# Optimization experiments

Measured on AMD Instinct MI355X. Metric: run time of the kernel, lower is better.

The kernel has to match this reference:

```python
import jax, jax.numpy as jnp
import numpy as np


def gcn_conv(x, edge_index, W, b):
    """GCNConv with add_self_loops + symmetric deg^-1/2 normalization, aggr='add'."""
    n = x.shape[0]
    self_loops = jnp.arange(n, dtype=edge_index.dtype)
    row = jnp.concatenate([edge_index[0], self_loops])  # source (j)
    col = jnp.concatenate([edge_index[1], self_loops])  # target (i)
    h = x @ W + b  # [N, out]
    deg = jax.ops.segment_sum(jnp.ones(row.shape, dtype=h.dtype), row, num_segments=n)
    dinv = jnp.where(deg > 0, deg ** -0.5, 0.0)
    norm = dinv[row] * dinv[col]  # [E+N]
    # out[i] = sum_{e: col_e = i} norm_e * h[row_e]
    return jax.ops.segment_sum(norm[:, None] * h[row], col, num_segments=n)


def setup_inputs() -> dict:
    key = jax.random.key(0)
    ks = jax.random.split(key, 5)
    N, E, D, K, C = 50000, 800000, 64, 500, 64
    x = jax.random.normal(ks[0], (N, D), dtype=jnp.float32)
    edge_index = jax.random.randint(ks[1], (2, E), 0, N, dtype=jnp.int32)
    W_embed = jax.random.normal(ks[2], (D, C), dtype=jnp.float32) * 0.1
    b_embed = jnp.zeros((C,), dtype=jnp.float32)
    W_assign = jax.random.normal(ks[3], (D, K), dtype=jnp.float32) * 0.1
    b_assign = jnp.zeros((K,), dtype=jnp.float32)
    return {"x": x, "edge_index": edge_index, "W_embed": W_embed, "b_embed": b_embed,
            "W_assign": W_assign, "b_assign": b_assign}


def reference(x, edge_index, W_embed, b_embed, W_assign, b_assign):
    n = x.shape[0]
    Z = gcn_conv(x, edge_index, W_embed, b_embed)                      # [N, C]
    S = jax.nn.softmax(gcn_conv(x, edge_index, W_assign, b_assign), -1)  # [N, K]
    next_X = S.T @ Z                                                    # [K, C]
    # next_A = S^T A S with A the (multi-)adjacency of the ORIGINAL edge_index
    # (to_dense_adj adds 1 at A[row_e, col_e]); computed sparsely:
    row, col = edge_index[0], edge_index[1]
    AS = jax.ops.segment_sum(S[col], row, num_segments=n)               # [N, K] = A @ S
    next_A = S.T @ AS                                                   # [K, K]
    return next_X, next_A
```

## Files before the change

### kernel.cpp

```cpp
#include <hip/hip_runtime.h>
#include <hip/hip_bf16.h>
#include <math.h>

#define DD 64
#define KK 500
#define KPAD 512
#define NPAD 50048
#define NS 50176
#define SLOTS 128
#define NBUCK 196
#define BCAP 6144

typedef __attribute__((ext_vector_type(8))) short bf16x8;
typedef __attribute__((ext_vector_type(4))) float f32x4;

#if defined(__has_builtin)
#if __has_builtin(__builtin_amdgcn_cvt_pk_f32_fp8) && __has_builtin(__builtin_amdgcn_cvt_pk_fp8_f32)
#define HAS_FP8_CVT 1
#endif
#endif

#ifdef HAS_FP8_CVT
#define F8_INV (1.0f / 256.f)
#else
#define F8_INV 0x1p112f
#endif

__device__ inline unsigned short f2bf(float f) {
    unsigned u = __float_as_uint(f);
    u += 0x7fffu + ((u >> 16) & 1u);
    return (unsigned short)(u >> 16);
}
__device__ inline unsigned packbf(float lo, float hi) {
    return ((unsigned)f2bf(hi) << 16) | (unsigned)f2bf(lo);
}
__device__ inline float bf2f(unsigned short h) {
    return __uint_as_float((unsigned)h << 16);
}

__device__ inline void gload_lds16(const void* g, void* l) {
    __builtin_amdgcn_global_load_lds(
        (const __attribute__((address_space(1))) unsigned int*)g,
        (__attribute__((address_space(3))) unsigned int*)l, 16, 0, 0);
}

#ifndef HAS_FP8_CVT
__device__ inline float f8bits(unsigned b) {
    return __uint_as_float(((b & 0x80u) << 24) | ((b & 0x7fu) << 20));
}
__device__ inline unsigned f32_to_fp8_slow(float f) {
    unsigned sgn = (__float_as_uint(f) >> 24) & 0x80u;
    float af = fabsf(f);
    if (!(af > 0.f)) return sgn;
    if (af >= 448.f) return sgn | 0x7E;
    int e; frexpf(af, &e);
    int E = e - 1 + 7;
    if (E < 1) { unsigned q = (unsigned)rintf(ldexpf(af, 9)); return sgn | q; }
    unsigned q = (unsigned)rintf(ldexpf(af, 10 - E));
    if (q >= 16) { q = 8; E++; }
    if (E > 15 || (E == 15 && q - 8 >= 7)) return sgn | 0x7E;
    return sgn | ((unsigned)E << 3) | (q - 8);
}
#endif

__device__ inline void accf8v4(float* a, uint4 v) {
#ifdef HAS_FP8_CVT
    auto f0 = __builtin_amdgcn_cvt_pk_f32_fp8(v.x, false);
    a[0] += f0[0]; a[1] += f0[1];
    auto f1 = __builtin_amdgcn_cvt_pk_f32_fp8(v.x, true);
    a[2] += f1[0]; a[3] += f1[1];
    auto f2 = __builtin_amdgcn_cvt_pk_f32_fp8(v.y, false);
    a[4] += f2[0]; a[5] += f2[1];
    auto f3 = __builtin_amdgcn_cvt_pk_f32_fp8(v.y, true);
    a[6] += f3[0]; a[7] += f3[1];
    auto f4 = __builtin_amdgcn_cvt_pk_f32_fp8(v.z, false);
    a[8] += f4[0]; a[9] += f4[1];
    auto f5 = __builtin_amdgcn_cvt_pk_f32_fp8(v.z, true);
    a[10] += f5[0]; a[11] += f5[1];
    auto f6 = __builtin_amdgcn_cvt_pk_f32_fp8(v.w, false);
    a[12] += f6[0]; a[13] += f6[1];
    auto f7 = __builtin_amdgcn_cvt_pk_f32_fp8(v.w, true);
    a[14] += f7[0]; a[15] += f7[1];
#else
    a[0]  += f8bits(v.x & 0xff);         a[1]  += f8bits((v.x >> 8) & 0xff);
    a[2]  += f8bits((v.x >> 16) & 0xff); a[3]  += f8bits((v.x >> 24) & 0xff);
    a[4]  += f8bits(v.y & 0xff);         a[5]  += f8bits((v.y >> 8) & 0xff);
    a[6]  += f8bits((v.y >> 16) & 0xff); a[7]  += f8bits((v.y >> 24) & 0xff);
    a[8]  += f8bits(v.z & 0xff);         a[9]  += f8bits((v.z >> 8) & 0xff);
    a[10] += f8bits((v.z >> 16) & 0xff); a[11] += f8bits((v.z >> 24) & 0xff);
    a[12] += f8bits(v.w & 0xff);         a[13] += f8bits((v.w >> 8) & 0xff);
    a[14] += f8bits((v.w >> 16) & 0xff); a[15] += f8bits((v.w >> 24) & 0xff);
#endif
}

__device__ inline void accbf4(float* a, uint2 v) {
    a[0] += __uint_as_float(v.x << 16);
    a[1] += __uint_as_float(v.x & 0xffff0000u);
    a[2] += __uint_as_float(v.y << 16);
    a[3] += __uint_as_float(v.y & 0xffff0000u);
}

__global__ void __launch_bounds__(256) binA_kernel(
        const int* __restrict__ rowv, const int* __restrict__ colv,
        int* __restrict__ bcurC, int* __restrict__ bcurR,
        int* __restrict__ bstoreC, unsigned char* __restrict__ bstoreR, int E) {
    __shared__ int hc[NBUCK], hr[NBUCK], baseC[NBUCK], baseR[NBUCK];
    int t = threadIdx.x;
    if (t < NBUCK) { hc[t] = 0; hr[t] = 0; }
    __syncthreads();
    int e0 = blockIdx.x * 1024 + t * 4;
    int r[4], c[4];
#pragma unroll
    for (int i = 0; i < 4; ++i) {
        int e = e0 + i;
        if (e < E) {
            r[i] = rowv[e];
            c[i] = colv[e];
            atomicAdd(&hc[c[i] >> 8], 1);
            atomicAdd(&hr[r[i] >> 8], 1);
        } else {
            r[i] = -1; c[i] = -1;
        }
    }
    __syncthreads();
    if (t < NBUCK) {
        baseC[t] = atomicAdd(&bcurC[t], hc[t]);
        baseR[t] = atomicAdd(&bcurR[t], hr[t]);
        hc[t] = 0; hr[t] = 0;
    }
    __syncthreads();
#pragma unroll
    for (int i = 0; i < 4; ++i) {
        if (r[i] >= 0) {
            int bc = c[i] >> 8;
            int oc = baseC[bc] + atomicAdd(&hc[bc], 1);
            if (oc < BCAP) bstoreC[bc * BCAP + oc] = (r[i] << 8) | (c[i] & 255);
            int br = r[i] >> 8;
            int orr = baseR[br] + atomicAdd(&hr[br], 1);
            if (orr < BCAP) bstoreR[br * BCAP + orr] = (unsigned char)(r[i] & 255);
        }
    }
}

__global__ void __launch_bounds__(256) buildcsr_kernel(
        const int* __restrict__ bcurC, const int* __restrict__ bstoreC,
        int* __restrict__ esrc, int* __restrict__ degc, int n) {
    __shared__ int cur[256];
    int b = blockIdx.x, t = threadIdx.x;
    cur[t] = 0;
    __syncthreads();
    int cnt = min(bcurC[b], BCAP);
    const int* src = bstoreC + b * BCAP;
    for (int i = t; i < cnt; i += 256) {
        int packed = src[i];
        int cl = packed & 255, rr = packed >> 8;
        int p = atomicAdd(&cur[cl], 1);
        if (p < SLOTS) esrc[((size_t)(b * 256 + cl) << 7) + p] = rr;
    }
    __syncthreads();
    int node = b * 256 + t;
    if (node < n) degc[node] = min(cur[t], SLOTS);
}

__global__ void __launch_bounds__(256) rowdeg_kernel(
        const int* __restrict__ bcurR, const unsigned char* __restrict__ bstoreR,
        float* __restrict__ dinv, int n) {
    __shared__ int cnt[256];
    int b = blockIdx.x, t = threadIdx.x;
    cnt[t] = 0;
    __syncthreads();
    int c = min(bcurR[b], BCAP);
    const unsigned char* src = bstoreR + b * BCAP;
    for (int i = t; i < c; i += 256) {
        atomicAdd(&cnt[src[i]], 1);
    }
    __syncthreads();
    int node = b * 256 + t;
    if (node < n) dinv[node] = 1.0f / sqrtf((float)(cnt[t] + 1));
}

__global__ void prep_kernel(const float* __restrict__ x, const float* __restrict__ dinv,
                            unsigned short* __restrict__ xb,
                            const float* __restrict__ Wa, const float* __restrict__ We,
                            unsigned short* __restrict__ WaT, unsigned short* __restrict__ WeT,
                            int n16) {
    int idx = blockIdx.x * blockDim.x + threadIdx.x;
    if (idx < n16) {
        int i = idx >> 4;
        float di = dinv[i];
        float4 v = ((const float4*)x)[idx];
        uint2 o;
        o.x = packbf(di * v.x, di * v.y);
        o.y = packbf(di * v.z, di * v.w);
        ((uint2*)xb)[idx] = o;
        return;
    }
    int j = idx - n16;
    if (j < KPAD * 64) {
        int c = j >> 6, d = j & 63;
        float v = (c < KK) ? Wa[(size_t)d * KK + c] : 0.f;
        WaT[j] = f2bf(v);
    } else if (j < (KPAD + DD) * 64) {
        int k = j - KPAD * 64;
        int c = k >> 6, d = k & 63;
        WeT[k] = f2bf(We[(size_t)d * 64 + c]);
    }
}

__global__ void agg_kernel(const unsigned short* __restrict__ xb, const float* __restrict__ dinv,
                           const int* __restrict__ degc, const int* __restrict__ esrc,
                           float* __restrict__ t, unsigned short* __restrict__ ub, int n) {
    int wv = (blockIdx.x * blockDim.x + threadIdx.x) >> 6;
    int ln = threadIdx.x & 63;
    int g = ln >> 4, q = ln & 15;
    if (wv >= NPAD) return;
    if (wv >= n) {
        if (g == 0) ((uint2*)ub)[(size_t)wv * 16 + q] = make_uint2(0u, 0u);
        return;
    }
    const uint2* X2 = (const uint2*)xb;
    float ac[4] = {0.f, 0.f, 0.f, 0.f};
    float ts = 0.f;
    if (g == 0) {
        uint2 v = X2[(size_t)wv * 16 + q];
        accbf4(ac, v);
    }
    int p = wv << 7;
    int pend = p + degc[wv];
    for (; p + 7 < pend; p += 8) {
        int s0 = esrc[p + g];
        int s1 = esrc[p + 4 + g];
        uint2 v0 = X2[(size_t)s0 * 16 + q];
        uint2 v1 = X2[(size_t)s1 * 16 + q];
        float w0 = dinv[s0], w1 = dinv[s1];
        accbf4(ac, v0); accbf4(ac, v1);
        ts += w0 + w1;
    }
    for (; p + 3 < pend; p += 4) {
        int s = esrc[p + g];
        uint2 v = X2[(size_t)s * 16 + q];
        ts += dinv[s];
        accbf4(ac, v);
    }
    if (g < pend - p) {
        int s = esrc[p + g];
        uint2 v = X2[(size_t)s * 16 + q];
        ts += dinv[s];
        accbf4(ac, v);
    }
#pragma unroll
    for (int j = 0; j < 4; ++j) {
        ac[j] += __shfl_xor(ac[j], 16, 64);
        ac[j] += __shfl_xor(ac[j], 32, 64);
    }
    ts += __shfl_xor(ts, 16, 64);
    ts += __shfl_xor(ts, 32, 64);
    if (g == 0) {
        uint2 o;
        o.x = packbf(ac[0], ac[1]);
        o.y = packbf(ac[2], ac[3]);
        ((uint2*)ub)[(size_t)wv * 16 + q] = o;
        if (q == 0) t[wv] = dinv[wv] + ts;
    }
}

#define F8ROW 520
__global__ void __launch_bounds__(256) fused_s3_kernel(
        const unsigned short* __restrict__ ub, const unsigned short* __restrict__ WaT,
        const unsigned short* __restrict__ WeT,
        const float* __restrict__ ba, const float* __restrict__ be,
        const float* __restrict__ dinv, const float* __restrict__ tsum,
        unsigned short* __restrict__ S_T, unsigned char* __restrict__ Sf8,
        unsigned short* __restrict__ Z_T, int n) {
    __shared__ float bs[512];
    __shared__ float bes[64];
    __shared__ float wmax[4][16];
    __shared__ float wsum[4][16];
    __shared__ unsigned char f8[16 * F8ROW];
    int t = threadIdx.x;
    int n0 = blockIdx.x * 16;
    {
        float b0 = (t * 2     < KK) ? ba[t * 2]     : 0.f;
        float b1 = (t * 2 + 1 < KK) ? ba[t * 2 + 1] : 0.f;
        bs[t * 2] = b0; bs[t * 2 + 1] = b1;
        if (t < 64) bes[t] = be[t];
    }
    __syncthreads();
    int wv = t >> 6, ln = t & 63;
    int nl = ln & 15;
    int g  = ln >> 4;
    int node = n0 + nl;
    int kb = wv * 128;
    float sd = (node < n) ? dinv[node] : 0.f;
    float st = (node < n) ? tsum[node] : 0.f;
    const unsigned short* brow = ub + (size_t)node * 64;
    bf16x8 bf0 = *(const bf16x8*)&brow[g * 8];
    bf16x8 bf1 = *(const bf16x8*)&brow[32 + g * 8];
    f32x4 acc[8];
#pragma unroll
    for (int mt = 0; mt < 8; ++mt) {
        const unsigned short* arow = WaT + (size_t)(kb + mt * 16 + nl) * 64;
        bf16x8 af0 = *(const bf16x8*)&arow[g * 8];
        bf16x8 af1 = *(const bf16x8*)&arow[32 + g * 8];
        f32x4 a = __builtin_amdgcn_mfma_f32_16x16x32_bf16(af0, bf0, (f32x4){0.f,0.f,0.f,0.f}, 0, 0, 0);
        acc[mt] = __builtin_amdgcn_mfma_f32_16x16x32_bf16(af1, bf1, a, 0, 0, 0);
    }
    float m = -1e30f;
#pragma unroll
    for (int mt = 0; mt < 8; ++mt) {
#pragma unroll
        for (int r = 0; r < 4; ++r) {
            int cl = kb + mt * 16 + g * 4 + r;
            float L = sd * (acc[mt][r] + st * bs[cl]);
            if (cl >= KK) L = -1e30f;
            acc[mt][r] = L;
            m = fmaxf(m, L);
        }
    }
    m = fmaxf(m, __shfl_xor(m, 16, 64));
    m = fmaxf(m, __shfl_xor(m, 32, 64));
    if (g == 0) wmax[wv][nl] = m;
    __syncthreads();
    m = fmaxf(fmaxf(wmax[0][nl], wmax[1][nl]), fmaxf(wmax[2][nl], wmax[3][nl]));
    float ssum = 0.f;
#pragma unroll
    for (int mt = 0; mt < 8; ++mt) {
#pragma unroll
        for (int r = 0; r < 4; ++r) {
            float e = expf(acc[mt][r] - m);
            acc[mt][r] = e;
            ssum += e;
        }
    }
    ssum += __shfl_xor(ssum, 16, 64);
    ssum += __shfl_xor(ssum, 32, 64);
    if (g == 0) wsum[wv][nl] = ssum;
    __syncthreads();
    float tot = (wsum[0][nl] + wsum[1][nl]) + (wsum[2][nl] + wsum[3][nl]);
    float rs = (node < n) ? (1.0f / tot) : 0.f;
    float sc = 256.f * rs;
    unsigned char* frow = &f8[nl * F8ROW];
#pragma unroll
    for (int mt = 0; mt < 8; ++mt) {
#pragma unroll
        for (int r = 0; r < 4; ++r) {
            int cl = kb + mt * 16 + g * 4 + r;
            S_T[(size_t)cl * NPAD + node] = f2bf(acc[mt][r] * rs);
        }
#ifdef HAS_FP8_CVT
        int pk = __builtin_amdgcn_cvt_pk_fp8_f32(acc[mt][0] * sc, acc[mt][1] * sc, 0, false);
        pk     = __builtin_amdgcn_cvt_pk_fp8_f32(acc[mt][2] * sc, acc[mt][3] * sc, pk, true);
#else
        int pk = (int)(f32_to_fp8_slow(acc[mt][0]*sc) | (f32_to_fp8_slow(acc[mt][1]*sc) << 8) |
                       (f32_to_fp8_slow(acc[mt][2]*sc) << 16) | (f32_to_fp8_slow(acc[mt][3]*sc) << 24));
#endif
        *(unsigned*)&frow[kb + mt * 16 + g * 4] = (unsigned)pk;
    }
    {
        const unsigned short* arow = WeT + (size_t)(wv * 16 + nl) * 64;
        bf16x8 af0 = *(const bf16x8*)&arow[g * 8];
        bf16x8 af1 = *(const bf16x8*)&arow[32 + g * 8];
        f32x4 a = __builtin_amdgcn_mfma_f32_16x16x32_bf16(af0, bf0, (f32x4){0.f,0.f,0.f,0.f}, 0, 0, 0);
        a = __builtin_amdgcn_mfma_f32_16x16x32_bf16(af1, bf1, a, 0, 0, 0);
#pragma unroll
        for (int r = 0; r < 4; ++r) {
            int ch = wv * 16 + g * 4 + r;
            float z = sd * (a[r] + st * bes[ch]);
            Z_T[(size_t)ch * NPAD + node] = f2bf(z);
        }
    }
    __syncthreads();
#pragma unroll
    for (int h = 0; h < 2; ++h) {
        int idx = t + h * 256;
        int row = idx >> 5;
        int off = (idx & 31) * 16;
        uint4 vv = *(const uint4*)&f8[row * F8ROW + off];
        int grow = n0 + row;
        if (grow < n) *(uint4*)&Sf8[(size_t)grow * KPAD + off] = vv;
    }
}

#define GT_ROWS 32
__global__ void __launch_bounds__(512) g_agg_t_kernel(
        const unsigned char* __restrict__ Sf8, const int* __restrict__ degc,
        const int* __restrict__ esrc, unsigned short* __restrict__ G_T, int n) {
    __shared__ unsigned short tl[GT_ROWS * 520];
    __shared__ int nextrow;
    int base = blockIdx.x * GT_ROWS;
    int ln = threadIdx.x & 63;
    int half = ln >> 5, lc = ln & 31;
    if (threadIdx.x == 0) nextrow = 0;
    __syncthreads();
    const uint4* S4 = (const uint4*)Sf8;
    const float inv = F8_INV;
    while (true) {
        int r = 0;
        if (ln == 0) r = atomicAdd(&nextrow, 1);
        r = __shfl(r, 0, 64);
        if (r >= GT_ROWS) break;
        int node = base + r;
        float a[16];
#pragma unroll
        for (int j = 0; j < 16; ++j) a[j] = 0.f;
        if (node < n) {
            int p = node << 7;
            int pend = p + degc[node];
            for (; p + 7 < pend; p += 8) {
                int s0 = esrc[p + half];
                int s1 = esrc[p + 2 + half];
                int s2 = esrc[p + 4 + half];
                int s3 = esrc[p + 6 + half];
                uint4 v0 = S4[(size_t)s0 * 32 + lc];
                uint4 v1 = S4[(size_t)s1 * 32 + lc];
                uint4 v2 = S4[(size_t)s2 * 32 + lc];
                uint4 v3 = S4[(size_t)s3 * 32 + lc];
                accf8v4(a, v0); accf8v4(a, v1); accf8v4(a, v2); accf8v4(a, v3);
            }
            for (; p + 1 < pend; p += 2) {
                int s = esrc[p + half];
                uint4 v = S4[(size_t)s * 32 + lc];
                accf8v4(a, v);
            }
            if (p < pend && half == 0) {
                int s = esrc[p];
                uint4 v = S4[(size_t)s * 32 + lc];
                accf8v4(a, v);
            }
        }
#pragma unroll
        for (int j = 0; j < 16; ++j) a[j] += __shfl_xor(a[j], 32, 64);
        uint4 o;
        if (half == 0) {
            o.x = packbf(a[0] * inv, a[1] * inv);
            o.y = packbf(a[2] * inv, a[3] * inv);
            o.z = packbf(a[4] * inv, a[5] * inv);
            o.w = packbf(a[6] * inv, a[7] * inv);
        } else {
            o.x = packbf(a[8]  * inv, a[9]  * inv);
            o.y = packbf(a[10] * inv, a[11] * inv);
            o.z = packbf(a[12] * inv, a[13] * inv);
            o.w = packbf(a[14] * inv, a[15] * inv);
        }
        *(uint4*)&tl[r * 520 + lc * 16 + half * 8] = o;
    }
    __syncthreads();
    {
        int k = threadIdx.x;
        unsigned wb[8];
#pragma unroll
        for (int j = 0; j < 8; ++j) {
            unsigned short lo = tl[(2 * j)     * 520 + k];
            unsigned short hi = tl[(2 * j + 1) * 520 + k];
            wb[j] = ((unsigned)hi << 16) | (unsigned)lo;
        }
        unsigned wc[8];
#pragma unroll
        for (int j = 0; j < 8; ++j) {
            unsigned short lo = tl[(16 + 2 * j) * 520 + k];
            unsigned short hi = tl[(17 + 2 * j) * 520 + k];
            wc[j] = ((unsigned)hi << 16) | (unsigned)lo;
        }
        size_t ob = (size_t)k * NPAD + base;
        *(uint4*)&G_T[ob]      = make_uint4(wb[0], wb[1], wb[2], wb[3]);
        *(uint4*)&G_T[ob + 8]  = make_uint4(wb[4], wb[5], wb[6], wb[7]);
        *(uint4*)&G_T[ob + 16] = make_uint4(wc[0], wc[1], wc[2], wc[3]);
        *(uint4*)&G_T[ob + 24] = make_uint4(wc[4], wc[5], wc[6], wc[7]);
    }
}

#define CPITCH 128
__global__ void __launch_bounds__(256) mfma_comb_kernel(
        const unsigned short* __restrict__ S_T, const unsigned short* __restrict__ G_T,
        const unsigned short* __restrict__ Z_T,
        float* __restrict__ partialA, float* __restrict__ partialX, int nPer) {
    __shared__ unsigned short Al[128 * 64];
    __shared__ unsigned short Bl[128 * 64];
    const int bid = blockIdx.x;
    const int kws = (bid & 7) * 115 + (bid >> 3);
    const int tile = kws % 20;
    const int zz   = kws / 20;
    const int t = threadIdx.x;
    const int ln = t & 63, wv = t >> 6;
    const int wa = (wv & 1) * 64, wb = (wv >> 1) * 64;
    const int lm = ln & 15, lk = (ln >> 4) * 8;
    const int nbeg = zz * nPer;
    const int nend = min(nbeg + nPer, NPAD);
    const bool isA = (tile < 16);
    const unsigned short* Ap = isA ? G_T : S_T;
    const unsigned short* Bp = isA ? S_T : Z_T;
    const int a0 = isA ? (tile >> 2) * 128 : (tile - 16) * 128;
    const int b0 = isA ? (tile & 3) * 128 : 0;
    float* op = isA ? (partialA + (size_t)zz * 512 * 512)
                    : (partialX + (size_t)zz * 512 * 128);
    const int ostride = isA ? 512 : 128;
    const int srow = ln >> 3;
    const int schunk = ((ln & 7) * 16) ^ (srow << 4);
    f32x4 acc[4][4];
#pragma unroll
    for (int i = 0; i < 4; ++i)
#pragma unroll
        for (int j = 0; j < 4; ++j) acc[i][j] = (f32x4){0.f, 0.f, 0.f, 0.f};
    for (int nb = nbeg; nb < nend; nb += 64) {
        __syncthreads();
#pragma unroll
        for (int j = 0; j < 4; ++j) {
            int rbase = (j * 4 + wv) * 8;
            int row = rbase + srow;
            const char* gA = (const char*)(Ap + (size_t)(a0 + row) * NPAD + nb) + schunk;
            const char* gB = (const char*)(Bp + (size_t)(b0 + row) * NPAD + nb) + schunk;
            gload_lds16(gA, (char*)Al + rbase * CPITCH);
            gload_lds16(gB, (char*)Bl + rbase * CPITCH);
        }
        __syncthreads();
#pragma unroll
        for (int ks = 0; ks < 64; ks += 32) {
            bf16x8 af[4], bfr[4];
#pragma unroll
            for (int i = 0; i < 4; ++i) {
                int rowA = wa + i * 16 + lm;
                af[i] = *(const bf16x8*)((const char*)Al + rowA * CPITCH
                        + (((ks + lk) * 2) ^ ((rowA & 7) << 4)));
            }
#pragma unroll
            for (int j = 0; j < 4; ++j) {
                int rowB = wb + j * 16 + lm;
                bfr[j] = *(const bf16x8*)((const char*)Bl + rowB * CPITCH
                         + (((ks + lk) * 2) ^ ((rowB & 7) << 4)));
            }
#pragma unroll
            for (int i = 0; i < 4; ++i)
#pragma unroll
                for (int j = 0; j < 4; ++j)
                    acc[i][j] = __builtin_amdgcn_mfma_f32_16x16x32_bf16(af[i], bfr[j], acc[i][j], 0, 0, 0);
        }
    }
#pragma unroll
    for (int i = 0; i < 4; ++i) {
#pragma unroll
        for (int j = 0; j < 4; ++j) {
            int bg = b0 + wb + j * 16 + lm;
#pragma unroll
            for (int r = 0; r < 4; ++r) {
                int ag = a0 + wa + i * 16 + (ln >> 4) * 4 + r;
                op[(size_t)ag * ostride + bg] = acc[i][j][r];
            }
        }
    }
}

__global__ void reduce2_kernel(const float* __restrict__ partialX, const float* __restrict__ partialA,
                               float* __restrict__ outX, float* __restrict__ outA, int Z) {
    int idx = blockIdx.x * blockDim.x + threadIdx.x;
    const int NX = KK * 64;
    if (idx < NX) {
        int a = idx >> 6, b = idx & 63;
        const float* p = partialX + (size_t)a * 128 + b;
        float s = 0.f;
        for (int z = 0; z < Z; ++z) s += p[(size_t)z * 512 * 128];
        outX[idx] = s;
        return;
    }
    int j = idx - NX;
    if (j >= KK * KK) return;
    int a = j / KK, b = j - a * KK;
    const float* p = partialA + (size_t)a * 512 + b;
    float s = 0.f;
    for (int z = 0; z < Z; ++z) s += p[(size_t)z * 512 * 512];
    outA[j] = s;
}

extern "C" void kernel_launch(void* const* d_in, const int* in_sizes, int n_in,
                              void* d_out, int out_size, void* d_ws, size_t ws_size,
                              hipStream_t stream) {
    const float* x        = (const float*)d_in[0];
    const int*   ei       = (const int*)d_in[1];
    const float* W_embed  = (const float*)d_in[2];
    const float* b_embed  = (const float*)d_in[3];
    const float* W_assign = (const float*)d_in[4];
    const float* b_assign = (const float*)d_in[5];

    const int N = in_sizes[0] / DD;
    const int E = in_sizes[1] / 2;
    const int C = in_sizes[3];
    const int K = in_sizes[5];

    const int* rowv = ei;
    const int* colv = ei + E;

    char* p = (char*)d_ws;
    auto alloc = [&](size_t bytes) -> void* {
        void* r = (void*)p;
        p += (bytes + 255) & ~(size_t)255;
        return r;
    };
    int*   bcur     = (int*)alloc((size_t)2 * NBUCK * 4);
    int*   bcurC    = bcur;
    int*   bcurR    = bcur + NBUCK;
    int*   bstoreC  = (int*)alloc((size_t)NBUCK * BCAP * 4);
    unsigned char* bstoreR = (unsigned char*)alloc((size_t)NBUCK * BCAP);
    int*   degc     = (int*)alloc((size_t)N * 4);
    float* dinv     = (float*)alloc((size_t)N * 4);
    float* tsum     = (float*)alloc((size_t)N * 4);
    int*   esrc     = (int*)alloc((size_t)NPAD * SLOTS * 4);
    float* u        = (float*)alloc((size_t)N * DD * 4);
    unsigned short* xb   = (unsigned short*)alloc((size_t)N * DD * 2);
    unsigned short* ubuf = (unsigned short*)alloc((size_t)NPAD * DD * 2);
    unsigned short* WaT  = (unsigned short*)alloc((size_t)KPAD * DD * 2);
    unsigned short* WeT  = (unsigned short*)alloc((size_t)DD * DD * 2);
    unsigned char*  Sf8  = (unsigned char*)alloc((size_t)N * KPAD);
    unsigned short* S_T  = (unsigned short*)alloc((size_t)KPAD * NPAD * 2);
    unsigned short* G_T  = (unsigned short*)alloc((size_t)KPAD * NPAD * 2);
    unsigned short* Z_T  = (unsigned short*)alloc((size_t)128 * NPAD * 2);

    const int nPer = 1088, ZSK = 46;
    float* partialA = (float*)alloc((size_t)ZSK * 512 * 512 * 4);
    float* partialX = (float*)u;

    float* outX = (float*)d_out;
    float* outA = outX + (size_t)K * C;

    (void)hipMemsetAsync(bcur, 0, (size_t)2 * NBUCK * 4, stream);

    binA_kernel<<<(E + 1023) / 1024, 256, 0, stream>>>(rowv, colv, bcurC, bcurR,
                                                       bstoreC, bstoreR, E);
    buildcsr_kernel<<<NBUCK, 256, 0, stream>>>(bcurC, bstoreC, esrc, degc, N);
    rowdeg_kernel<<<NBUCK, 256, 0, stream>>>(bcurR, bstoreR, dinv, N);

    {
        int total = N * 16 + (KPAD + DD) * 64;
        prep_kernel<<<(total + 255) / 256, 256, 0, stream>>>(x, dinv, xb, W_assign, W_embed,
                                                             WaT, WeT, N * 16);
    }

    agg_kernel<<<NPAD / 4, 256, 0, stream>>>(xb, dinv, degc, esrc, tsum, ubuf, N);

    fused_s3_kernel<<<NPAD / 16, 256, 0, stream>>>(ubuf, WaT, WeT, b_assign, b_embed,
                                                   dinv, tsum, S_T, Sf8, Z_T, N);

    g_agg_t_kernel<<<NPAD / GT_ROWS, 512, 0, stream>>>(Sf8, degc, esrc, G_T, N);

    mfma_comb_kernel<<<20 * ZSK, 256, 0, stream>>>(S_T, G_T, Z_T, partialA, partialX, nPer);

    {
        int total = K * C + K * K;
        reduce2_kernel<<<(total + 255) / 256, 256, 0, stream>>>(partialX, partialA, outX, outA, ZSK);
    }
}
```

Baseline: 345.8 us.

## Stage S_T transpose through LDS with 32-node blocks and split gather launch

fused_s3_kernel now handles 32 nodes per block with 512 threads. It stages the bf16 softmax output in a shared-memory tile and writes S_T as 16-byte coalesced chunks per row. Before, each thread did scattered 2-byte stores with a stride of NPAD. The g_agg_t gather kernel is also split into two launches over node halves, which adds one launch. Shared memory per block grows to about 50KB, which may reduce occupancy.

```diff
diff --git a/kernel.cpp b/kernel.cpp
--- a/kernel.cpp
+++ b/kernel.cpp
@@ -265,7 +265,7 @@
 }
 
 #define F8ROW 520
-__global__ void __launch_bounds__(256) fused_s3_kernel(
+__global__ void __launch_bounds__(512) fused_s3_kernel(
         const unsigned short* __restrict__ ub, const unsigned short* __restrict__ WaT,
         const unsigned short* __restrict__ WeT,
         const float* __restrict__ ba, const float* __restrict__ be,
@@ -274,25 +274,23 @@
         unsigned short* __restrict__ Z_T, int n) {
     __shared__ float bs[512];
     __shared__ float bes[64];
-    __shared__ float wmax[4][16];
-    __shared__ float wsum[4][16];
-    __shared__ unsigned char f8[16 * F8ROW];
+    __shared__ float wmax[2][4][16];
+    __shared__ float wsum[2][4][16];
+    __shared__ unsigned char f8[32 * F8ROW];
+    __shared__ unsigned short stile[512 * 32];
     int t = threadIdx.x;
-    int n0 = blockIdx.x * 16;
-    {
-        float b0 = (t * 2     < KK) ? ba[t * 2]     : 0.f;
-        float b1 = (t * 2 + 1 < KK) ? ba[t * 2 + 1] : 0.f;
-        bs[t * 2] = b0; bs[t * 2 + 1] = b1;
-        if (t < 64) bes[t] = be[t];
-    }
+    int n0 = blockIdx.x * 32;
+    bs[t] = (t < KK) ? ba[t] : 0.f;
+    if (t < 64) bes[t] = be[t];
     __syncthreads();
     int wv = t >> 6, ln = t & 63;
+    int wq = wv & 3, sub = wv >> 2;
     int nl = ln & 15;
     int g  = ln >> 4;
-    int node = n0 + nl;
-    int kb = wv * 128;
+    int node = n0 + sub * 16 + nl;
+    int kb = wq * 128;
     float sd = (node < n) ? dinv[node] : 0.f;
-    float st = (node < n) ? tsum[node] : 0.f;
+    float stv = (node < n) ? tsum[node] : 0.f;
     const unsigned short* brow = ub + (size_t)node * 64;
     bf16x8 bf0 = *(const bf16x8*)&brow[g * 8];
     bf16x8 bf1 = *(const bf16x8*)&brow[32 + g * 8];
@@ -311,7 +309,7 @@
 #pragma unroll
         for (int r = 0; r < 4; ++r) {
             int cl = kb + mt * 16 + g * 4 + r;
-            float L = sd * (acc[mt][r] + st * bs[cl]);
+            float L = sd * (acc[mt][r] + stv * bs[cl]);
             if (cl >= KK) L = -1e30f;
             acc[mt][r] = L;
             m = fmaxf(m, L);
@@ -319,9 +317,10 @@
     }
     m = fmaxf(m, __shfl_xor(m, 16, 64));
     m = fmaxf(m, __shfl_xor(m, 32, 64));
-    if (g == 0) wmax[wv][nl] = m;
-    __syncthreads();
-    m = fmaxf(fmaxf(wmax[0][nl], wmax[1][nl]), fmaxf(wmax[2][nl], wmax[3][nl]));
+    if (g == 0) wmax[sub][wq][nl] = m;
+    __syncthreads();
+    m = fmaxf(fmaxf(wmax[sub][0][nl], wmax[sub][1][nl]),
+              fmaxf(wmax[sub][2][nl], wmax[sub][3][nl]));
     float ssum = 0.f;
 #pragma unroll
     for (int mt = 0; mt < 8; ++mt) {
@@ -334,18 +333,18 @@
     }
     ssum += __shfl_xor(ssum, 16, 64);
     ssum += __shfl_xor(ssum, 32, 64);
-    if (g == 0) wsum[wv][nl] = ssum;
-    __syncthreads();
-    float tot = (wsum[0][nl] + wsum[1][nl]) + (wsum[2][nl] + wsum[3][nl]);
+    if (g == 0) wsum[sub][wq][nl] = ssum;
+    __syncthreads();
+    float tot = (wsum[sub][0][nl] + wsum[sub][1][nl]) + (wsum[sub][2][nl] + wsum[sub][3][nl]);
     float rs = (node < n) ? (1.0f / tot) : 0.f;
     float sc = 256.f * rs;
-    unsigned char* frow = &f8[nl * F8ROW];
+    unsigned char* frow = &f8[(sub * 16 + nl) * F8ROW];
 #pragma unroll
     for (int mt = 0; mt < 8; ++mt) {
 #pragma unroll
         for (int r = 0; r < 4; ++r) {
             int cl = kb + mt * 16 + g * 4 + r;
-            S_T[(size_t)cl * NPAD + node] = f2bf(acc[mt][r] * rs);
+            stile[cl * 32 + sub * 16 + nl] = f2bf(acc[mt][r] * rs);
         }
 #ifdef HAS_FP8_CVT
         int pk = __builtin_amdgcn_cvt_pk_fp8_f32(acc[mt][0] * sc, acc[mt][1] * sc, 0, false);
@@ -357,37 +356,44 @@
         *(unsigned*)&frow[kb + mt * 16 + g * 4] = (unsigned)pk;
     }
     {
-        const unsigned short* arow = WeT + (size_t)(wv * 16 + nl) * 64;
+        const unsigned short* arow = WeT + (size_t)(wq * 16 + nl) * 64;
         bf16x8 af0 = *(const bf16x8*)&arow[g * 8];
         bf16x8 af1 = *(const bf16x8*)&arow[32 + g * 8];
         f32x4 a = __builtin_amdgcn_mfma_f32_16x16x32_bf16(af0, bf0, (f32x4){0.f,0.f,0.f,0.f}, 0, 0, 0);
         a = __builtin_amdgcn_mfma_f32_16x16x32_bf16(af1, bf1, a, 0, 0, 0);
 #pragma unroll
         for (int r = 0; r < 4; ++r) {
-            int ch = wv * 16 + g * 4 + r;
-            float z = sd * (a[r] + st * bes[ch]);
+            int ch = wq * 16 + g * 4 + r;
+            float z = sd * (a[r] + stv * bes[ch]);
             Z_T[(size_t)ch * NPAD + node] = f2bf(z);
         }
     }
     __syncthreads();
 #pragma unroll
     for (int h = 0; h < 2; ++h) {
-        int idx = t + h * 256;
+        int idx = t + h * 512;
         int row = idx >> 5;
         int off = (idx & 31) * 16;
         uint4 vv = *(const uint4*)&f8[row * F8ROW + off];
         int grow = n0 + row;
         if (grow < n) *(uint4*)&Sf8[(size_t)grow * KPAD + off] = vv;
     }
+#pragma unroll
+    for (int h = 0; h < 4; ++h) {
+        int idx = t + h * 512;
+        int row = idx >> 2;
+        int c4 = (idx & 3) * 8;
+        *(uint4*)&S_T[(size_t)row * NPAD + n0 + c4] = *(const uint4*)&stile[row * 32 + c4];
+    }
 }
 
 #define GT_ROWS 32
 __global__ void __launch_bounds__(512) g_agg_t_kernel(
         const unsigned char* __restrict__ Sf8, const int* __restrict__ degc,
-        const int* __restrict__ esrc, unsigned short* __restrict__ G_T, int n) {
+        const int* __restrict__ esrc, unsigned short* __restrict__ G_T, int n, int node0) {
     __shared__ unsigned short tl[GT_ROWS * 520];
     __shared__ int nextrow;
-    int base = blockIdx.x * GT_ROWS;
+    int base = node0 + blockIdx.x * GT_ROWS;
     int ln = threadIdx.x & 63;
     int half = ln >> 5, lc = ln & 31;
     if (threadIdx.x == 0) nextrow = 0;
@@ -635,10 +641,14 @@
 
     agg_kernel<<<NPAD / 4, 256, 0, stream>>>(xb, dinv, degc, esrc, tsum, ubuf, N);
 
-    fused_s3_kernel<<<NPAD / 16, 256, 0, stream>>>(ubuf, WaT, WeT, b_assign, b_embed,
+    fused_s3_kernel<<<NPAD / 32, 512, 0, stream>>>(ubuf, WaT, WeT, b_assign, b_embed,
                                                    dinv, tsum, S_T, Sf8, Z_T, N);
 
-    g_agg_t_kernel<<<NPAD / GT_ROWS, 512, 0, stream>>>(Sf8, degc, esrc, G_T, N);
+    {
+        int halfN = NPAD / 2;
+        g_agg_t_kernel<<<halfN / GT_ROWS, 512, 0, stream>>>(Sf8, degc, esrc, G_T, N, 0);
+        g_agg_t_kernel<<<halfN / GT_ROWS, 512, 0, stream>>>(Sf8, degc, esrc, G_T, N, halfN);
+    }
 
     mfma_comb_kernel<<<20 * ZSK, 256, 0, stream>>>(S_T, G_T, Z_T, partialA, partialX, nPer);
 
```

Result: no change. 351.6 us (+1.7%).

## Double-buffer LDS tiles in MFMA combine kernel and split aggregation launch

Applied to the files above, without the earlier changes.

The combine GEMM kernel now keeps two LDS buffers and issues the async global-to-LDS loads for the next 64-column slab before computing on the current one. This is meant to hide global load latency behind MFMA work, at the cost of doubling LDS use per block, which may reduce occupancy. The G aggregation kernel is also split into two launches covering half the nodes each, which adds launch overhead and has no obvious speed intent. Both changes run with default settings.

```diff
diff --git a/kernel.cpp b/kernel.cpp
--- a/kernel.cpp
+++ b/kernel.cpp
@@ -384,10 +384,10 @@
 #define GT_ROWS 32
 __global__ void __launch_bounds__(512) g_agg_t_kernel(
         const unsigned char* __restrict__ Sf8, const int* __restrict__ degc,
-        const int* __restrict__ esrc, unsigned short* __restrict__ G_T, int n) {
+        const int* __restrict__ esrc, unsigned short* __restrict__ G_T, int n, int node0) {
     __shared__ unsigned short tl[GT_ROWS * 520];
     __shared__ int nextrow;
-    int base = blockIdx.x * GT_ROWS;
+    int base = node0 + blockIdx.x * GT_ROWS;
     int ln = threadIdx.x & 63;
     int half = ln >> 5, lc = ln & 31;
     if (threadIdx.x == 0) nextrow = 0;
@@ -470,12 +470,27 @@
 }
 
 #define CPITCH 128
+__device__ inline void stage_tiles(const unsigned short* Ap, const unsigned short* Bp,
+                                   int a0, int b0, int nb,
+                                   unsigned short* Albuf, unsigned short* Blbuf,
+                                   int wv, int srow, int schunk) {
+#pragma unroll
+    for (int j = 0; j < 4; ++j) {
+        int rbase = (j * 4 + wv) * 8;
+        int row = rbase + srow;
+        const char* gA = (const char*)(Ap + (size_t)(a0 + row) * NPAD + nb) + schunk;
+        const char* gB = (const char*)(Bp + (size_t)(b0 + row) * NPAD + nb) + schunk;
+        gload_lds16(gA, (char*)Albuf + rbase * CPITCH);
+        gload_lds16(gB, (char*)Blbuf + rbase * CPITCH);
+    }
+}
+
 __global__ void __launch_bounds__(256) mfma_comb_kernel(
         const unsigned short* __restrict__ S_T, const unsigned short* __restrict__ G_T,
         const unsigned short* __restrict__ Z_T,
         float* __restrict__ partialA, float* __restrict__ partialX, int nPer) {
-    __shared__ unsigned short Al[128 * 64];
-    __shared__ unsigned short Bl[128 * 64];
+    __shared__ unsigned short Al[2][128 * 64];
+    __shared__ unsigned short Bl[2][128 * 64];
     const int bid = blockIdx.x;
     const int kws = (bid & 7) * 115 + (bid >> 3);
     const int tile = kws % 20;
@@ -501,31 +516,28 @@
     for (int i = 0; i < 4; ++i)
 #pragma unroll
         for (int j = 0; j < 4; ++j) acc[i][j] = (f32x4){0.f, 0.f, 0.f, 0.f};
+    stage_tiles(Ap, Bp, a0, b0, nbeg, Al[0], Bl[0], wv, srow, schunk);
+    __syncthreads();
+    int cur = 0;
     for (int nb = nbeg; nb < nend; nb += 64) {
-        __syncthreads();
-#pragma unroll
-        for (int j = 0; j < 4; ++j) {
-            int rbase = (j * 4 + wv) * 8;
-            int row = rbase + srow;
-            const char* gA = (const char*)(Ap + (size_t)(a0 + row) * NPAD + nb) + schunk;
-            const char* gB = (const char*)(Bp + (size_t)(b0 + row) * NPAD + nb) + schunk;
-            gload_lds16(gA, (char*)Al + rbase * CPITCH);
-            gload_lds16(gB, (char*)Bl + rbase * CPITCH);
-        }
-        __syncthreads();
+        int nxt = nb + 64;
+        if (nxt < nend)
+            stage_tiles(Ap, Bp, a0, b0, nxt, Al[cur ^ 1], Bl[cur ^ 1], wv, srow, schunk);
+        const unsigned short* Ac = Al[cur];
+        const unsigned short* Bc = Bl[cur];
 #pragma unroll
         for (int ks = 0; ks < 64; ks += 32) {
             bf16x8 af[4], bfr[4];
 #pragma unroll
             for (int i = 0; i < 4; ++i) {
                 int rowA = wa + i * 16 + lm;
-                af[i] = *(const bf16x8*)((const char*)Al + rowA * CPITCH
+                af[i] = *(const bf16x8*)((const char*)Ac + rowA * CPITCH
                         + (((ks + lk) * 2) ^ ((rowA & 7) << 4)));
             }
 #pragma unroll
             for (int j = 0; j < 4; ++j) {
                 int rowB = wb + j * 16 + lm;
-                bfr[j] = *(const bf16x8*)((const char*)Bl + rowB * CPITCH
+                bfr[j] = *(const bf16x8*)((const char*)Bc + rowB * CPITCH
                          + (((ks + lk) * 2) ^ ((rowB & 7) << 4)));
             }
 #pragma unroll
@@ -534,6 +546,8 @@
                 for (int j = 0; j < 4; ++j)
                     acc[i][j] = __builtin_amdgcn_mfma_f32_16x16x32_bf16(af[i], bfr[j], acc[i][j], 0, 0, 0);
         }
+        __syncthreads();
+        cur ^= 1;
     }
 #pragma unroll
     for (int i = 0; i < 4; ++i) {
@@ -638,7 +652,11 @@
     fused_s3_kernel<<<NPAD / 16, 256, 0, stream>>>(ubuf, WaT, WeT, b_assign, b_embed,
                                                    dinv, tsum, S_T, Sf8, Z_T, N);
 
-    g_agg_t_kernel<<<NPAD / GT_ROWS, 512, 0, stream>>>(Sf8, degc, esrc, G_T, N);
+    {
+        int halfN = NPAD / 2;
+        g_agg_t_kernel<<<halfN / GT_ROWS, 512, 0, stream>>>(Sf8, degc, esrc, G_T, N, 0);
+        g_agg_t_kernel<<<halfN / GT_ROWS, 512, 0, stream>>>(Sf8, degc, esrc, G_T, N, halfN);
+    }
 
     mfma_comb_kernel<<<20 * ZSK, 256, 0, stream>>>(S_T, G_T, Z_T, partialA, partialX, nPer);
 
```

After: 348.7 us. Within noise of the previous version (+0.9%).
